# Optimization experiments

Measured on AMD Instinct MI355X. Metric: run time of the kernel, lower is better.

The kernel has to match this reference:

```python
import jax, jax.numpy as jnp
import numpy as np

N = 100000   # n_nodes
E = 1600000  # n_edges (avg degree 16)
IN, HID, OUT = 128, 128, 64


def setup_inputs() -> dict:
    key = jax.random.key(0)
    k0, k1, k2, k3 = jax.random.split(key, 4)
    x = jax.random.normal(k0, (N, IN), dtype=jnp.float32)
    edge_index = jax.random.randint(k1, (2, E), 0, N, dtype=jnp.int32)
    # Glorot-ish init for GCNConv weights, zero bias (PyG default bias=True)
    W1 = jax.random.normal(k2, (IN, HID), dtype=jnp.float32) * (1.0 / np.sqrt(IN))
    b1 = jnp.zeros((HID,), dtype=jnp.float32)
    W2 = jax.random.normal(k3, (HID, OUT), dtype=jnp.float32) * (1.0 / np.sqrt(HID))
    b2 = jnp.zeros((OUT,), dtype=jnp.float32)
    return {"x": x, "W1": W1, "b1": b1, "W2": W2, "b2": b2, "edge_index": edge_index}


def gcn_layer(x, W, b, src, dst):
    """PyG GCNConv: add self-loops, symmetric deg^{-1/2} normalization,
    linear transform, scatter-add aggregation at dst, plus bias."""
    n = x.shape[0]
    h = x @ W                                   # [n, d_out]
    loops = jnp.arange(n, dtype=src.dtype)
    s = jnp.concatenate([src, loops])           # sources incl. self-loops
    d = jnp.concatenate([dst, loops])           # targets incl. self-loops
    deg = jax.ops.segment_sum(jnp.ones_like(d, dtype=h.dtype), d, num_segments=n)
    dinv = jnp.where(deg > 0, jax.lax.rsqrt(deg), 0.0)
    norm = dinv[s] * dinv[d]                    # [E+n]
    msg = h[s] * norm[:, None]                  # gather + scale
    out = jax.ops.segment_sum(msg, d, num_segments=n)  # scatter-add
    return out + b


def reference(x, W1, b1, W2, b2, edge_index):
    src, dst = edge_index[0], edge_index[1]
    h = jax.nn.relu(gcn_layer(x, W1, b1, src, dst))
    return gcn_layer(h, W2, b2, src, dst)
```

## Files before the change

### kernel.cpp

```cpp
#include <hip/hip_runtime.h>

#define NNODES 100000
#define NEDGES 1600000
#define IND 128
#define HIDD 128
#define OUTD 64

#define BSHIFT 9
#define BSIZE  512
#define NBUCK  ((NNODES + BSIZE - 1) / BSIZE)
#define SLACK  9216
#define BIN_EPB  8192
#define SEG_CAP  10240
#define BINB   ((NEDGES + BIN_EPB - 1) / BIN_EPB)
#define WTB    ((IND * HIDD + HIDD * OUTD + 255) / 256)

typedef unsigned int  uint32;
typedef __attribute__((ext_vector_type(8))) short short8;
typedef __attribute__((ext_vector_type(4))) float floatx4;
typedef __attribute__((ext_vector_type(4))) unsigned int uivec4;
typedef __attribute__((ext_vector_type(4))) float fvec4;

__device__ __forceinline__ unsigned short f2bf(float f) {
    union { float f; uint32 u; } x; x.f = f;
    uint32 u = x.u;
    return (unsigned short)((u + 0x7fffu + ((u >> 16) & 1u)) >> 16);
}
__device__ __forceinline__ float bflo(uint32 u) {
    union { uint32 i; float f; } x; x.i = u << 16; return x.f;
}
__device__ __forceinline__ float bfhi(uint32 u) {
    union { uint32 i; float f; } x; x.i = u & 0xffff0000u; return x.f;
}

__global__ void k_bin(const int* __restrict__ src, const int* __restrict__ dst,
                      int* __restrict__ bcnt, uint32* __restrict__ staging, int e,
                      const float* __restrict__ W1, const float* __restrict__ W2,
                      unsigned short* __restrict__ wt1, unsigned short* __restrict__ wt2) {
    const int tid = threadIdx.x;
    if (blockIdx.x >= BINB) {
        int idx = (blockIdx.x - BINB) * 256 + tid;
        if (idx < IND * HIDD) {
            int k = idx / HIDD, m = idx - k * HIDD;
            wt1[m * IND + k] = f2bf(W1[idx]);
        } else {
            int j = idx - IND * HIDD;
            if (j < HIDD * OUTD) {
                int k = j / OUTD, m = j - k * OUTD;
                wt2[m * HIDD + k] = f2bf(W2[j]);
            }
        }
        return;
    }

    __shared__ int lh[NBUCK];
    __shared__ int lcur[NBUCK];
    for (int i = tid; i < NBUCK; i += 256) lh[i] = 0;
    __syncthreads();

    int start = blockIdx.x * BIN_EPB;
    int end = min(start + BIN_EPB, e);

    for (int i = start + tid; i < end; i += 256)
        atomicAdd(&lh[dst[i] >> BSHIFT], 1);
    __syncthreads();

    for (int i = tid; i < NBUCK; i += 256)
        lcur[i] = lh[i] ? atomicAdd(&bcnt[i], lh[i]) : 0;
    __syncthreads();

    for (int i = start + tid; i < end; i += 256) {
        int d = dst[i], s = src[i];
        int b = d >> BSHIFT;
        int pos = atomicAdd(&lcur[b], 1);
        if (pos < SLACK)
            staging[b * SLACK + pos] = ((uint32)(d & (BSIZE - 1)) << 17) | (uint32)s;
    }
}

__global__ void k_fill3(const uint32* __restrict__ staging, const int* __restrict__ bcnt,
                        int* __restrict__ row_ptr, int* __restrict__ csr_src,
                        float* __restrict__ dinv, int n) {
    __shared__ int nc[BSIZE];
    __shared__ int lcur[BSIZE];
    __shared__ int sbuf[256];
    __shared__ int boffl[NBUCK + 1];
    __shared__ int seg[SEG_CAP];
    const int b = blockIdx.x;
    const int base = b << BSHIFT;
    const int tid = threadIdx.x;
    const int nn = min(BSIZE, n - base);

    for (int i = tid; i < BSIZE; i += 256) nc[i] = 0;

    int vb = (tid < NBUCK) ? bcnt[tid] : 0;
    sbuf[tid] = vb;
    __syncthreads();
    for (int off = 1; off < 256; off <<= 1) {
        int t = (tid >= off) ? sbuf[tid - off] : 0;
        __syncthreads();
        sbuf[tid] += t;
        __syncthreads();
    }
    if (tid < NBUCK) boffl[tid] = sbuf[tid] - vb;
    if (tid == 255) boffl[NBUCK] = sbuf[255];
    __syncthreads();

    const uint32* st = staging + (size_t)b * SLACK;
    const int cnt = bcnt[b];
    for (int i = tid; i < cnt; i += 256)
        atomicAdd(&nc[st[i] >> 17], 1);
    __syncthreads();

    int a0 = nc[2 * tid], a1 = nc[2 * tid + 1];
    sbuf[tid] = a0 + a1;
    __syncthreads();
    for (int off = 1; off < 256; off <<= 1) {
        int t = (tid >= off) ? sbuf[tid - off] : 0;
        __syncthreads();
        sbuf[tid] += t;
        __syncthreads();
    }
    int ex = sbuf[tid] - (a0 + a1);
    const int r0 = boffl[b];
    if (2 * tid < nn) {
        row_ptr[base + 2 * tid] = r0 + ex;
        dinv[base + 2 * tid] = rsqrtf((float)(a0 + 1));
    }
    if (2 * tid + 1 < nn) {
        row_ptr[base + 2 * tid + 1] = r0 + ex + a0;
        dinv[base + 2 * tid + 1] = rsqrtf((float)(a1 + 1));
    }
    lcur[2 * tid] = ex;
    lcur[2 * tid + 1] = ex + a0;
    if (b == (int)gridDim.x - 1 && tid == 255) row_ptr[n] = boffl[NBUCK];
    __syncthreads();

    for (int i = tid; i < cnt; i += 256) {
        uint32 p = st[i];
        int dl = (int)(p >> 17);
        int s  = (int)(p & 0x1FFFFu);
        int pos = atomicAdd(&lcur[dl], 1);
        if (pos < SEG_CAP) seg[pos] = s;
        else               csr_src[r0 + pos] = s;
    }
    __syncthreads();
    int lim = min(cnt, SEG_CAP);
    for (int i = tid; i < lim; i += 256) csr_src[r0 + i] = seg[i];
}

template<int K, int M, bool ABF16>
__launch_bounds__(512)
__global__ void gemm_mfma(const void* __restrict__ Ap, const unsigned short* __restrict__ WT,
                          const float* __restrict__ dinv, unsigned short* __restrict__ C, int n) {
    constexpr int KP = K + 8;
    constexpr int NT = M / 16;
    __shared__ unsigned short Asl[128 * KP];
    __shared__ unsigned short Wsl[M * KP];

    const int tid = threadIdx.x;
    const int row0 = blockIdx.x * 128;

    {
        constexpr int SEG = (K * 2) / 16;
        const uint4* srcp = (const uint4*)WT;
        for (int idx = tid; idx < M * SEG; idx += 512) {
            int r = idx / SEG, s = idx - r * SEG;
            *(uint4*)(Wsl + r * KP + s * 8) = srcp[idx];
        }
    }
    if constexpr (ABF16) {
        constexpr int U4R = K / 8;
        const unsigned short* Ab = (const unsigned short*)Ap;
        for (int idx = tid; idx < 128 * U4R; idx += 512) {
            int r = idx / U4R, s = idx - r * U4R;
            int grow = row0 + r; if (grow >= n) grow = n - 1;
            *(uint4*)(Asl + r * KP + s * 8) = *(const uint4*)(Ab + (size_t)grow * K + s * 8);
        }
    } else {
        constexpr int F4R = K / 4;
        const float* Af = (const float*)Ap;
        for (int idx = tid; idx < 128 * F4R; idx += 512) {
            int r = idx / F4R, s = idx - r * F4R;
            int grow = row0 + r; if (grow >= n) grow = n - 1;
            float4 v = *(const float4*)(Af + (size_t)grow * K + s * 4);
            uint32 p0 = (uint32)f2bf(v.x) | ((uint32)f2bf(v.y) << 16);
            uint32 p1 = (uint32)f2bf(v.z) | ((uint32)f2bf(v.w) << 16);
            *(uint2*)(Asl + r * KP + s * 4) = make_uint2(p0, p1);
        }
    }
    __syncthreads();

    const int lane = tid & 63;
    const int wave = tid >> 6;
    const int mm = lane & 15;
    const int qq = lane >> 4;

    floatx4 acc[NT];
#pragma unroll
    for (int t = 0; t < NT; t++) acc[t] = (floatx4){0.f, 0.f, 0.f, 0.f};

#pragma unroll
    for (int kc = 0; kc < K / 32; kc++) {
        short8 a = *(const short8*)(Asl + (wave * 16 + mm) * KP + kc * 32 + qq * 8);
#pragma unroll
        for (int t = 0; t < NT; t++) {
            short8 b = *(const short8*)(Wsl + (t * 16 + mm) * KP + kc * 32 + qq * 8);
            acc[t] = __builtin_amdgcn_mfma_f32_16x16x32_bf16(a, b, acc[t], 0, 0, 0);
        }
    }

#pragma unroll
    for (int r = 0; r < 4; r++) {
        int grow = row0 + wave * 16 + qq * 4 + r;
        if (grow < n) {
            float dv = dinv[grow];
#pragma unroll
            for (int t = 0; t < NT; t++)
                C[(size_t)grow * M + t * 16 + mm] = f2bf(acc[t][r] * dv);
        }
    }
}

template<int M, bool RELU, bool OBF16>
__launch_bounds__(256)
__global__ void gather_k(const unsigned short* __restrict__ h,
                         const int* __restrict__ row_ptr,
                         const int* __restrict__ csr_src,
                         const float* __restrict__ dinv,
                         const float* __restrict__ bias,
                         void* __restrict__ outp, int n) {
    constexpr int LPG = M / 8;
    constexpr int GPB = 256 / LPG;
    const int g = threadIdx.x / LPG;
    const int l = threadIdx.x % LPG;
    const int v = blockIdx.x * GPB + g;
    if (v >= n) return;

    const float dv = dinv[v];
    float acc[8];
    {
        uint4 u = *(const uint4*)(h + (size_t)v * M + l * 8);
        acc[0] = bflo(u.x); acc[1] = bfhi(u.x);
        acc[2] = bflo(u.y); acc[3] = bfhi(u.y);
        acc[4] = bflo(u.z); acc[5] = bfhi(u.z);
        acc[6] = bflo(u.w); acc[7] = bfhi(u.w);
    }

    int j   = row_ptr[v];
    int end = row_ptr[v + 1];
    for (; j + 3 < end; j += 4) {
        int s0 = csr_src[j];
        int s1 = csr_src[j + 1];
        int s2 = csr_src[j + 2];
        int s3 = csr_src[j + 3];
        uint4 u0 = *(const uint4*)(h + (size_t)s0 * M + l * 8);
        uint4 u1 = *(const uint4*)(h + (size_t)s1 * M + l * 8);
        uint4 u2 = *(const uint4*)(h + (size_t)s2 * M + l * 8);
        uint4 u3 = *(const uint4*)(h + (size_t)s3 * M + l * 8);
        acc[0] += (bflo(u0.x) + bflo(u1.x)) + (bflo(u2.x) + bflo(u3.x));
        acc[1] += (bfhi(u0.x) + bfhi(u1.x)) + (bfhi(u2.x) + bfhi(u3.x));
        acc[2] += (bflo(u0.y) + bflo(u1.y)) + (bflo(u2.y) + bflo(u3.y));
        acc[3] += (bfhi(u0.y) + bfhi(u1.y)) + (bfhi(u2.y) + bfhi(u3.y));
        acc[4] += (bflo(u0.z) + bflo(u1.z)) + (bflo(u2.z) + bflo(u3.z));
        acc[5] += (bfhi(u0.z) + bfhi(u1.z)) + (bfhi(u2.z) + bfhi(u3.z));
        acc[6] += (bflo(u0.w) + bflo(u1.w)) + (bflo(u2.w) + bflo(u3.w));
        acc[7] += (bfhi(u0.w) + bfhi(u1.w)) + (bfhi(u2.w) + bfhi(u3.w));
    }
    for (; j < end; j++) {
        int s0 = csr_src[j];
        uint4 u0 = *(const uint4*)(h + (size_t)s0 * M + l * 8);
        acc[0] += bflo(u0.x); acc[1] += bfhi(u0.x);
        acc[2] += bflo(u0.y); acc[3] += bfhi(u0.y);
        acc[4] += bflo(u0.z); acc[5] += bfhi(u0.z);
        acc[6] += bflo(u0.w); acc[7] += bfhi(u0.w);
    }

#pragma unroll
    for (int i = 0; i < 8; i++) {
        acc[i] = acc[i] * dv + bias[l * 8 + i];
        if (RELU) acc[i] = fmaxf(acc[i], 0.0f);
    }

    if constexpr (OBF16) {
        uivec4 p;
#pragma unroll
        for (int c = 0; c < 4; c++)
            p[c] = (uint32)f2bf(acc[2 * c]) | ((uint32)f2bf(acc[2 * c + 1]) << 16);
        __builtin_nontemporal_store(p,
            (uivec4*)((unsigned short*)outp + (size_t)v * M + l * 8));
    } else {
        float* op = (float*)outp + (size_t)v * M + l * 8;
        fvec4 a0 = {acc[0], acc[1], acc[2], acc[3]};
        fvec4 a1 = {acc[4], acc[5], acc[6], acc[7]};
        __builtin_nontemporal_store(a0, (fvec4*)op);
        __builtin_nontemporal_store(a1, (fvec4*)(op + 4));
    }
}

extern "C" void kernel_launch(void* const* d_in, const int* in_sizes, int n_in,
                              void* d_out, int out_size, void* d_ws, size_t ws_size,
                              hipStream_t stream) {
    const float* x  = (const float*)d_in[0];
    const float* W1 = (const float*)d_in[1];
    const float* b1 = (const float*)d_in[2];
    const float* W2 = (const float*)d_in[3];
    const float* b2 = (const float*)d_in[4];
    const int*   ei = (const int*)d_in[5];
    const int* src = ei;
    const int* dst = ei + NEDGES;
    float* out = (float*)d_out;

    char* ws = (char*)d_ws;
    float*  dinv    = (float*)ws;   ws += (size_t)NNODES * 4;
    int*    row_ptr = (int*)ws;     ws += (size_t)(NNODES + 4) * 4;
    int*    bcnt    = (int*)ws;     ws += 256 * 4;
    int*    boff    = (int*)ws;     ws += 260 * 4;
    unsigned short* wt1 = (unsigned short*)ws;  ws += (size_t)IND * HIDD * 2;
    unsigned short* wt2 = (unsigned short*)ws;  ws += (size_t)HIDD * OUTD * 2;
    int*    csr_src = (int*)ws;     ws += (size_t)NEDGES * 4;
    uint32* staging = (uint32*)ws;  ws += (size_t)NBUCK * SLACK * 4;
    unsigned short* hr  = (unsigned short*)ws;  ws += (size_t)NNODES * HIDD * 2;
    unsigned short* hbf = (unsigned short*)ws;

    hipMemsetAsync(bcnt, 0, 256 * 4, stream);
    k_bin<<<BINB + WTB, 256, 0, stream>>>(src, dst, bcnt, staging, NEDGES, W1, W2, wt1, wt2);
    k_fill3<<<NBUCK, 256, 0, stream>>>(staging, bcnt, row_ptr, csr_src, dinv, NNODES);

    gemm_mfma<IND, HIDD, false><<<(NNODES + 127) / 128, 512, 0, stream>>>(
        x, wt1, dinv, hbf, NNODES);
    gather_k<HIDD, true, true><<<(NNODES * (HIDD / 8) + 255) / 256, 256, 0, stream>>>(
        hbf, row_ptr, csr_src, dinv, b1, hr, NNODES);

    gemm_mfma<HIDD, OUTD, true><<<(NNODES + 127) / 128, 512, 0, stream>>>(
        hr, wt2, dinv, hbf, NNODES);
    gather_k<OUTD, false, false><<<(NNODES * (OUTD / 8) + 255) / 256, 256, 0, stream>>>(
        hbf, row_ptr, csr_src, dinv, b2, out, NNODES);
}
```

Before: 316.8 us.

## Fuse layer-1 aggregation with layer-2 GEMM in one kernel

Adds a gather_gemm kernel that aggregates layer-1 neighbor features for 16 nodes per block, applies bias and ReLU, stages the bf16 result in LDS, and immediately multiplies it by W2 with MFMA. This removes the intermediate hidden-activation buffer write/read and one kernel launch. In exchange, every block reloads W2 into shared memory and the block must sync between gather and GEMM, with small 16-node tiles.

```diff
diff --git a/kernel.cpp b/kernel.cpp
--- a/kernel.cpp
+++ b/kernel.cpp
@@ -218,6 +218,112 @@
 #pragma unroll
             for (int t = 0; t < NT; t++)
                 C[(size_t)grow * M + t * 16 + mm] = f2bf(acc[t][r] * dv);
+        }
+    }
+}
+
+__launch_bounds__(256)
+__global__ void gather_gemm(const unsigned short* __restrict__ h,
+                            const int* __restrict__ row_ptr,
+                            const int* __restrict__ csr_src,
+                            const float* __restrict__ dinv,
+                            const float* __restrict__ bias1,
+                            const unsigned short* __restrict__ WT2,
+                            unsigned short* __restrict__ C2, int n) {
+    constexpr int K  = HIDD;
+    constexpr int KP = K + 8;
+    constexpr int M2 = OUTD;
+    __shared__ unsigned short Atl[16 * KP];
+    __shared__ unsigned short Wsl[M2 * KP];
+
+    const int tid = threadIdx.x;
+
+    {
+        constexpr int SEG = (K * 2) / 16;
+        const uint4* srcp = (const uint4*)WT2;
+        for (int idx = tid; idx < M2 * SEG; idx += 256) {
+            int r = idx / SEG, s = idx - r * SEG;
+            *(uint4*)(Wsl + r * KP + s * 8) = srcp[idx];
+        }
+    }
+
+    const int g = tid >> 4;
+    const int l = tid & 15;
+    const int v0 = blockIdx.x * 16;
+    const int v = v0 + g;
+
+    uint4 pk = make_uint4(0u, 0u, 0u, 0u);
+    if (v < n) {
+        const float dv = dinv[v];
+        float acc[8];
+        {
+            uint4 u = *(const uint4*)(h + (size_t)v * K + l * 8);
+            acc[0] = bflo(u.x); acc[1] = bfhi(u.x);
+            acc[2] = bflo(u.y); acc[3] = bfhi(u.y);
+            acc[4] = bflo(u.z); acc[5] = bfhi(u.z);
+            acc[6] = bflo(u.w); acc[7] = bfhi(u.w);
+        }
+
+        int j   = row_ptr[v];
+        int end = row_ptr[v + 1];
+        for (; j + 3 < end; j += 4) {
+            int s0 = csr_src[j];
+            int s1 = csr_src[j + 1];
+            int s2 = csr_src[j + 2];
+            int s3 = csr_src[j + 3];
+            uint4 u0 = *(const uint4*)(h + (size_t)s0 * K + l * 8);
+            uint4 u1 = *(const uint4*)(h + (size_t)s1 * K + l * 8);
+            uint4 u2 = *(const uint4*)(h + (size_t)s2 * K + l * 8);
+            uint4 u3 = *(const uint4*)(h + (size_t)s3 * K + l * 8);
+            acc[0] += (bflo(u0.x) + bflo(u1.x)) + (bflo(u2.x) + bflo(u3.x));
+            acc[1] += (bfhi(u0.x) + bfhi(u1.x)) + (bfhi(u2.x) + bfhi(u3.x));
+            acc[2] += (bflo(u0.y) + bflo(u1.y)) + (bflo(u2.y) + bflo(u3.y));
+            acc[3] += (bfhi(u0.y) + bfhi(u1.y)) + (bfhi(u2.y) + bfhi(u3.y));
+            acc[4] += (bflo(u0.z) + bflo(u1.z)) + (bflo(u2.z) + bflo(u3.z));
+            acc[5] += (bfhi(u0.z) + bfhi(u1.z)) + (bfhi(u2.z) + bfhi(u3.z));
+            acc[6] += (bflo(u0.w) + bflo(u1.w)) + (bflo(u2.w) + bflo(u3.w));
+            acc[7] += (bfhi(u0.w) + bfhi(u1.w)) + (bfhi(u2.w) + bfhi(u3.w));
+        }
+        for (; j < end; j++) {
+            int s0 = csr_src[j];
+            uint4 u0 = *(const uint4*)(h + (size_t)s0 * K + l * 8);
+            acc[0] += bflo(u0.x); acc[1] += bfhi(u0.x);
+            acc[2] += bflo(u0.y); acc[3] += bfhi(u0.y);
+            acc[4] += bflo(u0.z); acc[5] += bfhi(u0.z);
+            acc[6] += bflo(u0.w); acc[7] += bfhi(u0.w);
+        }
+
+#pragma unroll
+        for (int i = 0; i < 8; i++) {
+            acc[i] = fmaxf(acc[i] * dv + bias1[l * 8 + i], 0.0f);
+        }
+        pk.x = (uint32)f2bf(acc[0]) | ((uint32)f2bf(acc[1]) << 16);
+        pk.y = (uint32)f2bf(acc[2]) | ((uint32)f2bf(acc[3]) << 16);
+        pk.z = (uint32)f2bf(acc[4]) | ((uint32)f2bf(acc[5]) << 16);
+        pk.w = (uint32)f2bf(acc[6]) | ((uint32)f2bf(acc[7]) << 16);
+    }
+    *(uint4*)(Atl + g * KP + l * 8) = pk;
+    __syncthreads();
+
+    const int lane = tid & 63;
+    const int wv = tid >> 6;
+    const int mm = lane & 15;
+    const int qq = lane >> 4;
+
+    floatx4 o = (floatx4){0.f, 0.f, 0.f, 0.f};
+#pragma unroll
+    for (int kc = 0; kc < K / 32; kc++) {
+        short8 a = *(const short8*)(Atl + mm * KP + kc * 32 + qq * 8);
+        short8 b = *(const short8*)(Wsl + (wv * 16 + mm) * KP + kc * 32 + qq * 8);
+        o = __builtin_amdgcn_mfma_f32_16x16x32_bf16(a, b, o, 0, 0, 0);
+    }
+
+#pragma unroll
+    for (int r = 0; r < 4; r++) {
+        int grow = v0 + qq * 4 + r;
+        if (grow < n) {
+            float dv2 = dinv[grow];
+            C2[(size_t)grow * M2 + wv * 16 + mm] = f2bf(o[r] * dv2);
         }
     }
 }
@@ -320,20 +426,19 @@
     unsigned short* wt2 = (unsigned short*)ws;  ws += (size_t)HIDD * OUTD * 2;
     int*    csr_src = (int*)ws;     ws += (size_t)NEDGES * 4;
     uint32* staging = (uint32*)ws;  ws += (size_t)NBUCK * SLACK * 4;
-    unsigned short* hr  = (unsigned short*)ws;  ws += (size_t)NNODES * HIDD * 2;
-    unsigned short* hbf = (unsigned short*)ws;
+    unsigned short* hbf1 = (unsigned short*)ws; ws += (size_t)NNODES * HIDD * 2;
+    unsigned short* hbf2 = (unsigned short*)ws;
 
     hipMemsetAsync(bcnt, 0, 256 * 4, stream);
     k_bin<<<BINB + WTB, 256, 0, stream>>>(src, dst, bcnt, staging, NEDGES, W1, W2, wt1, wt2);
     k_fill3<<<NBUCK, 256, 0, stream>>>(staging, bcnt, row_ptr, csr_src, dinv, NNODES);
 
     gemm_mfma<IND, HIDD, false><<<(NNODES + 127) / 128, 512, 0, stream>>>(
-        x, wt1, dinv, hbf, NNODES);
-    gather_k<HIDD, true, true><<<(NNODES * (HIDD / 8) + 255) / 256, 256, 0, stream>>>(
-        hbf, row_ptr, csr_src, dinv, b1, hr, NNODES);
-
-    gemm_mfma<HIDD, OUTD, true><<<(NNODES + 127) / 128, 512, 0, stream>>>(
-        hr, wt2, dinv, hbf, NNODES);
+        x, wt1, dinv, hbf1, NNODES);
+
+    gather_gemm<<<(NNODES + 15) / 16, 256, 0, stream>>>(
+        hbf1, row_ptr, csr_src, dinv, b1, wt2, hbf2, NNODES);
+
     gather_k<OUTD, false, false><<<(NNODES * (OUTD / 8) + 255) / 256, 256, 0, stream>>>(
-        hbf, row_ptr, csr_src, dinv, b2, out, NNODES);
-}
+        hbf2, row_ptr, csr_src, dinv, b2, out, NNODES);
+}
```

Measured after the change: 306.9 us. -3.2%, faster.
